# Performance work log

Measured on AMD Instinct MI355X. Metric: run time of the kernel, lower is better.

The kernel has to match this reference:

```python
import jax, jax.numpy as jnp
import numpy as np
import math

B, S, D, H = 4, 1024, 1024, 16
DK = D // H
K_INDEX = 5


def setup_inputs() -> dict:
    key = jax.random.key(0)
    ks = jax.random.split(key, 10)
    s = 0.02
    return {
        "query": jax.random.normal(ks[0], (B, S, D), jnp.float32),
        "key": jax.random.normal(ks[1], (B, S, D), jnp.float32),
        "values": jax.random.normal(ks[2], (B, S, D), jnp.float32),
        "lens": jax.random.randint(ks[3], (B,), 0, S),
        "Wq": jax.random.normal(ks[4], (D, D), jnp.float32) * s,  # shared q/k proj (kq_same=True)
        "bq": jnp.zeros((D,), jnp.float32),
        "Wv": jax.random.normal(ks[5], (D, D), jnp.float32) * s,
        "bv": jnp.zeros((D,), jnp.float32),
        "Wo": jax.random.normal(ks[6], (D, D), jnp.float32) * s,
        "bo": jnp.zeros((D,), jnp.float32),
        "gammas": jax.random.normal(ks[7], (H, 1, 1), jnp.float32) * 0.1,
        "ln_w": jnp.ones((D,), jnp.float32),
        "ln_b": jnp.zeros((D,), jnp.float32),
    }


def _split_heads(x):
    b, s, _ = x.shape
    return x.reshape(b, s, H, DK).transpose(0, 2, 1, 3)  # [B,H,S,DK]


def reference(query, key, values, lens, Wq, bq, Wv, bv, Wo, bo, gammas, ln_w, ln_b):
    # causal mask, peek_cur=False -> strict lower triangle; eval mode (no random masking)
    mask = jnp.tril(jnp.ones((S, S), bool), -1)[None, None]  # [1,1,S,S]

    q = _split_heads(query @ Wq.T + bq)
    k = _split_heads(key @ Wq.T + bq)   # kq_same: shared weights
    v = _split_heads(values @ Wv.T + bv)

    scores = jnp.einsum("bhid,bhjd->bhij", q, k) / math.sqrt(DK)
    NEG = jnp.finfo(scores.dtype).min

    # --- distance-decay term (no_grad in torch -> stop_gradient) ---
    s_ = jax.nn.softmax(jnp.where(mask, scores, NEG), axis=-1)
    distcum = jnp.cumsum(s_, axis=-1)
    disttotal = jnp.sum(s_, axis=-1, keepdims=True)
    idx = jnp.arange(S, dtype=scores.dtype)
    pos_effect = jnp.abs(idx[None, :] - idx[:, None])[None, None]  # |j - i|
    dist = jnp.sqrt(jnp.clip((disttotal - distcum) * pos_effect, 0.0, None))
    dist = jax.lax.stop_gradient(dist)

    gam = -jnp.abs(gammas)[None]  # [1,H,1,1]
    total_effect = jnp.clip(jnp.exp(dist * gam), 1e-5, 1e5)
    scores = scores * total_effect

    scores = jnp.where(mask, scores, NEG)
    p = jax.nn.softmax(scores, axis=-1)
    p = jnp.where(mask, p, 0.0)

    # maxout rescale (peek_cur=False)
    scale = jnp.minimum(1.0 / jnp.max(p, axis=-1, keepdims=True), 5.0)
    p = p * scale

    attn = jnp.einsum("bhij,bhjd->bhid", p, v)
    concat = attn.transpose(0, 2, 1, 3).reshape(B, S, D)
    attn_out = concat @ Wo.T + bo

    # k_select sparsification of the (post-softmax, maxout-scaled) scores
    sc_a = p[:, :, :K_INDEX, :]
    sc_b = p[:, :, K_INDEX:, :]
    kth = jax.lax.top_k(sc_b, K_INDEX)[0][..., -1:]  # k-th largest per row
    sc_b = jnp.where(sc_b >= kth, sc_b, NEG)
    sparse_scores = jax.nn.softmax(jnp.concatenate([sc_a, sc_b], axis=2), axis=-1)

    # residual (eval: dropout is identity) + LayerNorm
    y = query + attn_out
    mu = jnp.mean(y, axis=-1, keepdims=True)
    var = jnp.mean((y - mu) ** 2, axis=-1, keepdims=True)
    out = (y - mu) / jnp.sqrt(var + 1e-5) * ln_w + ln_b
    return (out, sparse_scores)
```

## Files before the change

### kernel.cpp

```cpp
#include <hip/hip_runtime.h>
#include <hip/hip_fp16.h>

#define Ssz 1024
#define Dsz 1024
#define Hsz 16
#define DKsz 64
#define Bsz 4
#define NEGI (-1.0e30f)
#define NEGD (-1.0e300)

typedef float f32x4 __attribute__((ext_vector_type(4)));
typedef float f32x2 __attribute__((ext_vector_type(2)));
typedef _Float16 f16x8 __attribute__((ext_vector_type(8)));
typedef _Float16 f16x4 __attribute__((ext_vector_type(4)));
typedef _Float16 f16x2 __attribute__((ext_vector_type(2)));

__device__ __forceinline__ float wmaxf(float x) {
#pragma unroll
  for (int o = 32; o; o >>= 1) x = fmaxf(x, __shfl_xor(x, o));
  return x;
}
__device__ __forceinline__ float wsumf(float x) {
#pragma unroll
  for (int o = 32; o; o >>= 1) x += __shfl_xor(x, o);
  return x;
}
__device__ __forceinline__ double wmaxd(double x) {
#pragma unroll
  for (int o = 32; o; o >>= 1) x = fmax(x, __shfl_xor(x, o));
  return x;
}
__device__ __forceinline__ double wsumd(double x) {
#pragma unroll
  for (int o = 32; o; o >>= 1) x += __shfl_xor(x, o);
  return x;
}
__device__ __forceinline__ int wmini(int x) {
#pragma unroll
  for (int o = 32; o; o >>= 1) x = min(x, __shfl_xor(x, o));
  return x;
}
__device__ __forceinline__ int sswz(int c) { return c ^ (((c >> 5) & 7) << 2); }
__device__ __forceinline__ int pswz(int c, int r) { return c ^ (r & 7) ^ ((c >> 3) & 7); }

__global__ __launch_bounds__(256) void wsplit_qv(
    const float* __restrict__ Wq, const float* __restrict__ Wv,
    __half* __restrict__ wqhi, __half* __restrict__ wqlo, __half* __restrict__ wvhi) {
  const size_t i = ((size_t)blockIdx.x * 256 + threadIdx.x) * 4;
  const f32x4 q = *(const f32x4*)(Wq + i);
  const f32x4 v = *(const f32x4*)(Wv + i);
  f16x4 hq, lq, hv;
#pragma unroll
  for (int e = 0; e < 4; e++) {
    const _Float16 h = (_Float16)q[e];
    hq[e] = h;
    lq[e] = (_Float16)(q[e] - (float)h);
    hv[e] = (_Float16)v[e];
  }
  *(f16x4*)((_Float16*)wqhi + i) = hq;
  *(f16x4*)((_Float16*)wqlo + i) = lq;
  *(f16x4*)((_Float16*)wvhi + i) = hv;
}

__global__ __launch_bounds__(256) void wsplit_o(
    const float* __restrict__ Wo, __half* __restrict__ wohi) {
  const size_t i = ((size_t)blockIdx.x * 256 + threadIdx.x) * 4;
  const f32x4 v = *(const f32x4*)(Wo + i);
  f16x4 hv;
#pragma unroll
  for (int e = 0; e < 4; e++) hv[e] = (_Float16)v[e];
  *(f16x4*)((_Float16*)wohi + i) = hv;
}

__global__ __launch_bounds__(256) void asplit_hl(
    const float* __restrict__ A, __half* __restrict__ hi, __half* __restrict__ lo) {
  const size_t i = ((size_t)blockIdx.x * 256 + threadIdx.x) * 4;
  const f32x4 v = *(const f32x4*)(A + i);
  f16x4 h, l;
#pragma unroll
  for (int e = 0; e < 4; e++) {
    const _Float16 hh = (_Float16)v[e];
    h[e] = hh;
    l[e] = (_Float16)(v[e] - (float)hh);
  }
  *(f16x4*)((_Float16*)hi + i) = h;
  *(f16x4*)((_Float16*)lo + i) = l;
}

__global__ __launch_bounds__(256) void asplit_h(
    const float* __restrict__ A, __half* __restrict__ hi) {
  const size_t i = ((size_t)blockIdx.x * 256 + threadIdx.x) * 4;
  const f32x4 v = *(const f32x4*)(A + i);
  f16x4 h;
#pragma unroll
  for (int e = 0; e < 4; e++) h[e] = (_Float16)v[e];
  *(f16x4*)((_Float16*)hi + i) = h;
}

__global__ __launch_bounds__(256) void gemm_qk(
    const __half* __restrict__ Ahi, const __half* __restrict__ Alo,
    const __half* __restrict__ wqhi, const __half* __restrict__ wqlo,
    const float* __restrict__ bias, __half* __restrict__ ohi, __half* __restrict__ olo) {
  const int w = threadIdx.x >> 6, lane = threadIdx.x & 63;
  const int quad = lane >> 4, l16 = lane & 15;
  const int m0 = blockIdx.x * 64 + w * 16;
  const int n0 = blockIdx.y * 64;
  f32x4 acc[4] = {};
  const size_t arow = (size_t)(m0 + l16) * Dsz;
  for (int k0 = 0; k0 < Dsz; k0 += 32) {
    const f16x8 ahi = *(const f16x8*)((const _Float16*)Ahi + arow + k0 + quad * 8);
    const f16x8 alo = *(const f16x8*)((const _Float16*)Alo + arow + k0 + quad * 8);
#pragma unroll
    for (int t = 0; t < 4; t++) {
      const size_t woff = (size_t)(n0 + t * 16 + l16) * Dsz + k0 + quad * 8;
      const f16x8 whi = *(const f16x8*)((const _Float16*)wqhi + woff);
      const f16x8 wlo = *(const f16x8*)((const _Float16*)wqlo + woff);
      acc[t] = __builtin_amdgcn_mfma_f32_16x16x32_f16(ahi, whi, acc[t], 0, 0, 0);
      acc[t] = __builtin_amdgcn_mfma_f32_16x16x32_f16(ahi, wlo, acc[t], 0, 0, 0);
      acc[t] = __builtin_amdgcn_mfma_f32_16x16x32_f16(alo, whi, acc[t], 0, 0, 0);
    }
  }
#pragma unroll
  for (int t = 0; t < 4; t++) {
    const int oc = n0 + t * 16 + l16;
    const float bv = bias[oc];
    const int hh = oc >> 6, dk = oc & 63;
#pragma unroll
    for (int r = 0; r < 4; r++) {
      const int mr = m0 + quad * 4 + r;
      const int bb = mr >> 10, ss = mr & 1023;
      const float v = acc[t][r] + bv;
      const size_t idx = ((size_t)(bb * Hsz + hh) * Ssz + ss) * DKsz + dk;
      const __half h = __float2half(v);
      ohi[idx] = h;
      olo[idx] = __float2half(v - __half2float(h));
    }
  }
}

__global__ __launch_bounds__(256) void gemm_v(
    const __half* __restrict__ Ahi, const __half* __restrict__ wvhi,
    const float* __restrict__ bias, __half* __restrict__ out_t) {
  const int w = threadIdx.x >> 6, lane = threadIdx.x & 63;
  const int quad = lane >> 4, l16 = lane & 15;
  const int m0 = blockIdx.x * 64 + w * 16;
  const int n0 = blockIdx.y * 64;
  f32x4 acc[4] = {};
  const size_t arow = (size_t)(m0 + l16) * Dsz;
  for (int k0 = 0; k0 < Dsz; k0 += 32) {
    const f16x8 ahi = *(const f16x8*)((const _Float16*)Ahi + arow + k0 + quad * 8);
#pragma unroll
    for (int t = 0; t < 4; t++) {
      const size_t woff = (size_t)(n0 + t * 16 + l16) * Dsz + k0 + quad * 8;
      const f16x8 whi = *(const f16x8*)((const _Float16*)wvhi + woff);
      acc[t] = __builtin_amdgcn_mfma_f32_16x16x32_f16(ahi, whi, acc[t], 0, 0, 0);
    }
  }
#pragma unroll
  for (int t = 0; t < 4; t++) {
    const int oc = n0 + t * 16 + l16;
    const float bv = bias[oc];
    const int hh = oc >> 6, dk = oc & 63;
#pragma unroll
    for (int r = 0; r < 4; r++) {
      const int mr = m0 + quad * 4 + r;
      const int bb = mr >> 10, ss = mr & 1023;
      out_t[((size_t)(bb * Hsz + hh) * DKsz + dk) * Ssz + ss] = __float2half(acc[t][r] + bv);
    }
  }
}

__global__ __launch_bounds__(256) void gemm_o(
    const __half* __restrict__ A, const __half* __restrict__ wohi,
    const float* __restrict__ bias, float* __restrict__ outf) {
  const int w = threadIdx.x >> 6, lane = threadIdx.x & 63;
  const int quad = lane >> 4, l16 = lane & 15;
  const int m0 = blockIdx.x * 64 + w * 16;
  const int n0 = blockIdx.y * 64;
  f32x4 acc[4] = {};
  const size_t arow = (size_t)(m0 + l16) * Dsz;
  for (int k0 = 0; k0 < Dsz; k0 += 32) {
    const f16x8 a = *(const f16x8*)(A + arow + k0 + quad * 8);
#pragma unroll
    for (int t = 0; t < 4; t++) {
      const size_t woff = (size_t)(n0 + t * 16 + l16) * Dsz + k0 + quad * 8;
      const f16x8 whi = *(const f16x8*)((const _Float16*)wohi + woff);
      acc[t] = __builtin_amdgcn_mfma_f32_16x16x32_f16(a, whi, acc[t], 0, 0, 0);
    }
  }
#pragma unroll
  for (int t = 0; t < 4; t++) {
    const int oc = n0 + t * 16 + l16;
    const float bv = bias[oc];
#pragma unroll
    for (int r = 0; r < 4; r++) {
      const int mr = m0 + quad * 4 + r;
      outf[(size_t)mr * Dsz + oc] = acc[t][r] + bv;
    }
  }
}


__global__ __launch_bounds__(256) void attn_scores(
    const __half* __restrict__ qhi, const __half* __restrict__ qlo,
    const __half* __restrict__ khi, const __half* __restrict__ klo,
    float* __restrict__ scores, int bh0) {
  const int w = threadIdx.x >> 6, lane = threadIdx.x & 63;
  const int quad = lane >> 4, l16 = lane & 15;
  const int lbh = blockIdx.y, bh = bh0 + lbh;
  for (int cc = 0; cc < 2; cc++) {
    const int chunk = cc ? (63 - (int)blockIdx.x) : (int)blockIdx.x;
    const int i0 = chunk * 16;
    const size_t qb = ((size_t)bh * Ssz + i0 + l16) * DKsz + quad * 8;
    const f16x8 ah0 = *(const f16x8*)(qhi + qb);
    const f16x8 ah1 = *(const f16x8*)(qhi + qb + 32);
    const f16x8 al0 = *(const f16x8*)(qlo + qb);
    const f16x8 al1 = *(const f16x8*)(qlo + qb + 32);
    float* dst = scores + ((size_t)lbh * Ssz + i0) * Ssz;
    for (int tt = 0; tt < 16; tt++) {
      const int n0 = (w + tt * 4) * 16;
      if (n0 > i0 + 14) continue;
      const size_t kb = ((size_t)bh * Ssz + n0 + l16) * DKsz + quad * 8;
      const f16x8 bh0v = *(const f16x8*)(khi + kb);
      const f16x8 bh1v = *(const f16x8*)(khi + kb + 32);
      const f16x8 bl0v = *(const f16x8*)(klo + kb);
      const f16x8 bl1v = *(const f16x8*)(klo + kb + 32);
      f32x4 accs = {};
      accs = __builtin_amdgcn_mfma_f32_16x16x32_f16(al0, bl0v, accs, 0, 0, 0);
      accs = __builtin_amdgcn_mfma_f32_16x16x32_f16(al1, bl1v, accs, 0, 0, 0);
      accs = __builtin_amdgcn_mfma_f32_16x16x32_f16(ah0, bl0v, accs, 0, 0, 0);
      accs = __builtin_amdgcn_mfma_f32_16x16x32_f16(ah1, bl1v, accs, 0, 0, 0);
      accs = __builtin_amdgcn_mfma_f32_16x16x32_f16(al0, bh0v, accs, 0, 0, 0);
      accs = __builtin_amdgcn_mfma_f32_16x16x32_f16(al1, bh1v, accs, 0, 0, 0);
      accs = __builtin_amdgcn_mfma_f32_16x16x32_f16(ah0, bh0v, accs, 0, 0, 0);
      accs = __builtin_amdgcn_mfma_f32_16x16x32_f16(ah1, bh1v, accs, 0, 0, 0);
#pragma unroll
      for (int r = 0; r < 4; r++)
        dst[(size_t)(quad * 4 + r) * Ssz + n0 + l16] = accs[r] * 0.125f;
    }
  }
}

__global__ __launch_bounds__(256) void attn_soft(
    float* __restrict__ scores, const float* __restrict__ gam,
    float* __restrict__ sparse, int bh0) {
  const int w = threadIdx.x >> 6, lane = threadIdx.x & 63;
  const int lbh = blockIdx.y, bh = bh0 + lbh;
  const int hidx = bh & 15;
  const float gf = -fabsf(gam[hidx]);
  const int jb = 2 * lane;
  for (int cc = 0; cc < 2; cc++) {
    const int chunk = cc ? (63 - (int)blockIdx.x) : (int)blockIdx.x;
    const int i0 = chunk * 16;
    for (int rr = 0; rr < 4; rr++) {
      const int gi = i0 + w * 4 + rr;
      const int nch = __builtin_amdgcn_readfirstlane((gi + 127) >> 7);
      float* rowp = scores + ((size_t)lbh * Ssz + gi) * Ssz;
      float xf[16];
      float m1 = NEGI;
#pragma unroll
      for (int e = 0; e < 8; e++) {
        if (e < nch) {
          const int j0 = 128 * e + jb;
          const f32x2 t = *(const f32x2*)(rowp + j0);
          xf[2 * e] = t[0];
          xf[2 * e + 1] = t[1];
          if (j0 < gi) m1 = fmaxf(m1, t[0]);
          if (j0 + 1 < gi) m1 = fmaxf(m1, t[1]);
        }
      }
      m1 = wmaxf(m1);
      float s[16];
#pragma unroll
      for (int k = 0; k < 16; k++) s[k] = 0.f;
#pragma unroll
      for (int e = 0; e < 8; e++) {
        if (e < nch) {
          const int j0 = 128 * e + jb;
          if (j0 < gi) s[2 * e] = __expf(xf[2 * e] - m1);
          if (j0 + 1 < gi) s[2 * e + 1] = __expf(xf[2 * e + 1] - m1);
        }
      }
      float tot[8];
#pragma unroll
      for (int e = 0; e < 8; e++) {
        if (e < nch) {
          const float q2 = s[2 * e] + s[2 * e + 1];
          float v = __shfl_down(q2, 1);
          if (lane == 63) v = 0.f;
#pragma unroll
          for (int o = 1; o < 64; o <<= 1) {
            const float t = __shfl_down(v, o);
            if (lane + o < 64) v += t;
          }
          tot[e] = __shfl(q2 + v, 0);
          const float t1 = v;
          const float t0e = v + s[2 * e + 1];
          s[2 * e] = t0e;
          s[2 * e + 1] = t1;
        }
      }
      float csum = 0.f;
#pragma unroll
      for (int e = 7; e >= 0; e--) {
        if (e < nch) {
          s[2 * e] += csum;
          s[2 * e + 1] += csum;
          csum += tot[e];
        }
      }
      const float ls = csum;
      const float invls = (ls > 0.f) ? 1.0f / ls : 0.f;
      float ys[16];
      float m2 = NEGI;
#pragma unroll
      for (int k = 0; k < 16; k++) ys[k] = NEGI;
#pragma unroll
      for (int e = 0; e < 8; e++) {
        if (e < nch) {
#pragma unroll
          for (int i = 0; i < 2; i++) {
            const int j = 128 * e + jb + i;
            if (j < gi) {
              const float pe = (float)(gi - j);
              const float tn = s[2 * e + i] * invls;
              const float tl = tn > 0.f ? tn * pe : 0.f;
              float te = __expf(gf * sqrtf(tl));
              te = te < 1e-5f ? 1e-5f : te;
              const float vv = xf[2 * e + i] * te;
              ys[2 * e + i] = vv;
              m2 = fmaxf(m2, vv);
            }
          }
        }
      }
      m2 = wmaxf(m2);
      float xs[16];
#pragma unroll
      for (int k = 0; k < 16; k++) xs[k] = 0.f;
      float ls3 = 0.f, mev = 0.f;
#pragma unroll
      for (int e = 0; e < 8; e++) {
        if (e < nch) {
#pragma unroll
          for (int i = 0; i < 2; i++) {
            const int j = 128 * e + jb + i;
            if (j < gi) {
              const float ev = __expf(ys[2 * e + i] - m2);
              xs[2 * e + i] = ev;
              ls3 += ev;
              mev = fmaxf(mev, ev);
            }
          }
        }
      }
      ls3 = wsumf(ls3);
      mev = wmaxf(mev);
      const float inv2 = (ls3 > 0.f) ? 1.0f / ls3 : 0.f;
      const float mp = mev * inv2;
      const float scl = (mp > 0.f) ? fminf(1.0f / mp, 5.0f) : 5.0f;
      const float c2 = inv2 * scl;
#pragma unroll
      for (int k = 0; k < 16; k++) xs[k] *= c2;
      const float m3 = mp * scl;
      {
        _Float16* prow = (_Float16*)rowp;
#pragma unroll
        for (int e = 0; e < 8; e++) {
          f16x2 hp;
          hp[0] = (_Float16)xs[2 * e];
          hp[1] = (_Float16)xs[2 * e + 1];
          *(f16x2*)(prow + 128 * e + jb) = hp;
        }
      }

      float* dst = sparse + ((size_t)bh * Ssz + gi) * Ssz;
      if (gi < 5) {
        float o4[16];
        float ls4 = 0.f;
#pragma unroll
        for (int k = 0; k < 16; k++) {
          const float ev = expf(xs[k] - m3);
          o4[k] = ev;
          ls4 += ev;
        }
        const float inv3 = 1.0f / fmaxf(wsumf(ls4), 1e-30f);
#pragma unroll
        for (int e = 0; e < 8; e++) {
          f32x2 st;
          st[0] = o4[2 * e] * inv3;
          st[1] = o4[2 * e + 1] * inv3;
          *(f32x2*)(dst + 128 * e + jb) = st;
        }
      } else {
        float m5 = 0.f, m6 = 0.f;
        {
          unsigned int removed = 0;
          for (int r6 = 0; r6 < 6; r6++) {
            float lm = NEGI;
#pragma unroll
            for (int k = 0; k < 16; k++)
              if (!((removed >> k) & 1)) lm = fmaxf(lm, ys[k]);
            const float m = wmaxf(lm);
            const unsigned long long bal = __ballot(lm == m);
            const int src = __ffsll(bal) - 1;
            int rem_k = 0;
#pragma unroll
            for (int k = 15; k >= 0; k--)
              if (!((removed >> k) & 1) && ys[k] == m) rem_k = k;
            if (lane == src) removed |= 1u << rem_k;
            if (r6 == 4) m5 = m;
            if (r6 == 5) m6 = m;
          }
        }
        const float bstar = 0.5f * (m5 + m6);
        const float ETA = 6e-5f;
        const float wlo = m6 - 0.1f, whi = m5 + 0.1f;
        float md[16];
        float mn = 0.f;
#pragma unroll
        for (int e = 0; e < 8; e++) {
          md[2 * e] = 0.f;
          md[2 * e + 1] = 0.f;
          if (e < nch) {
#pragma unroll
            for (int i = 0; i < 2; i++) {
              const int j = 128 * e + jb + i;
              const int k = 2 * e + i;
              if (j < gi && ys[k] >= wlo && ys[k] <= whi) {
                const float pe = (float)(gi - j);
                const float t0 = fmaxf(s[k] * invls, 0.f);
                float telo = __expf(gf * sqrtf(fmaxf(t0 - ETA, 0.f) * pe));
                telo = fminf(fmaxf(telo, 1e-5f), 1.0f);
                float tehi = __expf(gf * sqrtf((t0 + ETA) * pe));
                tehi = fminf(fmaxf(tehi, 1e-5f), 1.0f);
                md[k] = fminf(fabsf(xf[k]) * (telo - tehi) + 2e-4f, 0.04f);
                mn = fmaxf(mn, md[k]);
              }
            }
          }
        }
        mn = wmaxf(mn);
        float cnt = 0.f;
        unsigned int mK = 0, mA = 0;
#pragma unroll
        for (int e = 0; e < 8; e++) {
          if (e < nch) {
#pragma unroll
            for (int i = 0; i < 2; i++) {
              const int j = 128 * e + jb + i;
              const int k = 2 * e + i;
              if (j < gi) {
                const float margin = fminf(1.5f * (md[k] + mn) + 1e-4f, 0.06f);
                if (ys[k] > bstar + margin) {
                  mK |= 1u << k; cnt += 1.f;
                } else if (!(ys[k] < bstar - margin)) {
                  mA |= 1u << k; cnt += 2048.f;
                }
              }
            }
          }
        }
        cnt = wsumf(cnt);
        const float cA = floorf(cnt * (1.0f / 2048.0f));
        const float cK = cnt - 2048.0f * cA;
        float vvf[16];
        float vK = 0.f, vA = 0.f;
#pragma unroll
        for (int k = 0; k < 16; k++) {
          vvf[k] = 0.f;
          if (((mK | mA) >> k) & 1) {
            const float val = __expf(xs[k] - m3);
            vvf[k] = val;
            if ((mK >> k) & 1) vK += val; else vA += val;
          }
        }
        vK = wsumf(vK); vA = wsumf(vA);
        const float vbar = (cA > 0.5f) ? vA / cA : 0.f;
        const float Zhat = vK + (5.0f - cK) * vbar;
        const float invZ = (Zhat > 0.f) ? 1.0f / Zhat : 0.f;
#pragma unroll
        for (int e = 0; e < 8; e++) {
          f32x2 st;
#pragma unroll
          for (int i = 0; i < 2; i++) {
            const int k = 2 * e + i;
            const bool isK = (mK >> k) & 1;
            const bool isA = (mA >> k) & 1;
            st[i] = isK ? vvf[k] * invZ : isA ? 0.5f * vvf[k] * invZ : 0.f;
          }
          *(f32x2*)(dst + 128 * e + jb) = st;
        }
      }
    }
  }
}

__global__ __launch_bounds__(256) void attn_pv(
    const float* __restrict__ scoresP, const __half* __restrict__ vt,
    __half* __restrict__ attn_c, int bh0) {
  const int w = threadIdx.x >> 6, lane = threadIdx.x & 63;
  const int quad = lane >> 4, l16 = lane & 15;
  const int lbh = blockIdx.y, bh = bh0 + lbh;
  const int hidx = bh & 15, bidx = bh >> 4;
  const _Float16* pb = (const _Float16*)scoresP;
  const int dk0 = w * 16;
  for (int cc = 0; cc < 2; cc++) {
    const int chunk = cc ? (63 - (int)blockIdx.x) : (int)blockIdx.x;
    const int i0 = chunk * 16;
    const int kmax = (i0 + 15 + 31) & ~31;
    f32x4 acc = {};
    const size_t prow = ((size_t)lbh * Ssz + i0 + l16) * 2048;
    const size_t vrow = ((size_t)bh * DKsz + dk0 + l16) * Ssz;
    for (int k0 = 0; k0 < kmax; k0 += 32) {
      const f16x8 a = *(const f16x8*)(pb + prow + k0 + quad * 8);
      const f16x8 b = *(const f16x8*)(vt + vrow + k0 + quad * 8);
      acc = __builtin_amdgcn_mfma_f32_16x16x32_f16(a, b, acc, 0, 0, 0);
    }
#pragma unroll
    for (int r = 0; r < 4; r++) {
      const int ss = i0 + quad * 4 + r;
      attn_c[((size_t)bidx * Ssz + ss) * Dsz + hidx * DKsz + dk0 + l16] = __float2half(acc[r]);
    }
  }
}

__global__ __launch_bounds__(256) void attn_kernel(
    const __half* __restrict__ qhi, const __half* __restrict__ qlo,
    const __half* __restrict__ khi, const __half* __restrict__ klo,
    const __half* __restrict__ vt, const float* __restrict__ gam,
    __half* __restrict__ attn_c, float* __restrict__ sparse) {
  __shared__ __align__(16) float sc[16 * 1024];
  const int w = threadIdx.x >> 6, lane = threadIdx.x & 63;
  const int quad = lane >> 4, l16 = lane & 15;
  const int bh = blockIdx.y, i0 = blockIdx.x * 16;
  const int hidx = bh & 15, bidx = bh >> 4;
  _Float16* pbase = (_Float16*)sc;

  {
    const size_t qb = ((size_t)bh * Ssz + i0 + l16) * DKsz + quad * 8;
    const f16x8 ah0 = *(const f16x8*)(qhi + qb);
    const f16x8 ah1 = *(const f16x8*)(qhi + qb + 32);
    const f16x8 al0 = *(const f16x8*)(qlo + qb);
    const f16x8 al1 = *(const f16x8*)(qlo + qb + 32);
    for (int tt = 0; tt < 16; tt++) {
      const int n0 = (w + tt * 4) * 16;
      const size_t kb = ((size_t)bh * Ssz + n0 + l16) * DKsz + quad * 8;
      const f16x8 bh0 = *(const f16x8*)(khi + kb);
      const f16x8 bh1 = *(const f16x8*)(khi + kb + 32);
      const f16x8 bl0 = *(const f16x8*)(klo + kb);
      const f16x8 bl1 = *(const f16x8*)(klo + kb + 32);
      f32x4 accs = {};
      accs = __builtin_amdgcn_mfma_f32_16x16x32_f16(al0, bl0, accs, 0, 0, 0);
      accs = __builtin_amdgcn_mfma_f32_16x16x32_f16(al1, bl1, accs, 0, 0, 0);
      accs = __builtin_amdgcn_mfma_f32_16x16x32_f16(ah0, bl0, accs, 0, 0, 0);
      accs = __builtin_amdgcn_mfma_f32_16x16x32_f16(ah1, bl1, accs, 0, 0, 0);
      accs = __builtin_amdgcn_mfma_f32_16x16x32_f16(al0, bh0, accs, 0, 0, 0);
      accs = __builtin_amdgcn_mfma_f32_16x16x32_f16(al1, bh1, accs, 0, 0, 0);
      accs = __builtin_amdgcn_mfma_f32_16x16x32_f16(ah0, bh0, accs, 0, 0, 0);
      accs = __builtin_amdgcn_mfma_f32_16x16x32_f16(ah1, bh1, accs, 0, 0, 0);
      const int pc = sswz(n0 + l16);
#pragma unroll
      for (int r = 0; r < 4; r++)
        sc[(quad * 4 + r) * 1024 + pc] = accs[r] * 0.125f;
    }
  }
  __syncthreads();

  {
    const double g = -fabs((double)gam[hidx]);
    for (int rr = 0; rr < 4; rr++) {
      const int r = w * 4 + rr, gi = i0 + r;
      float xf[16];
#pragma unroll
// ... 203 lines not shown
      const f16x8 a = *(const f16x8*)(pbase + l16 * 2048 + pswz(cch, l16) * 8);
      const f16x8 b =
          *(const f16x8*)(vt + ((size_t)bh * DKsz + dk0 + l16) * Ssz + k0 + quad * 8);
      acc = __builtin_amdgcn_mfma_f32_16x16x32_f16(a, b, acc, 0, 0, 0);
    }
#pragma unroll
    for (int r = 0; r < 4; r++) {
      const int ss = i0 + quad * 4 + r;
      attn_c[((size_t)bidx * Ssz + ss) * Dsz + hidx * DKsz + dk0 + l16] = __float2half(acc[r]);
    }
  }
}

__global__ __launch_bounds__(256) void ln_kernel(
    const float* __restrict__ query, const float* __restrict__ attn_out,
    const float* __restrict__ ln_w, const float* __restrict__ ln_b,
    float* __restrict__ out) {
  __shared__ float red[8];
  const int n = blockIdx.x, t = threadIdx.x;
  const int w = t >> 6, lane = t & 63;
  float y[4];
  float s = 0.f, s2 = 0.f;
#pragma unroll
  for (int k = 0; k < 4; k++) {
    const int j = t + k * 256;
    const float v = query[(size_t)n * Dsz + j] + attn_out[(size_t)n * Dsz + j];
    y[k] = v;
    s += v;
    s2 += v * v;
  }
  s = wsumf(s);
  s2 = wsumf(s2);
  if (lane == 0) { red[w] = s; red[4 + w] = s2; }
  __syncthreads();
  s = red[0] + red[1] + red[2] + red[3];
  s2 = red[4] + red[5] + red[6] + red[7];
  const float mu = s * (1.0f / 1024.0f);
  const float var = fmaxf(s2 * (1.0f / 1024.0f) - mu * mu, 0.0f);
  const float rs = rsqrtf(var + 1e-5f);
#pragma unroll
  for (int k = 0; k < 4; k++) {
    const int j = t + k * 256;
    out[(size_t)n * Dsz + j] = (y[k] - mu) * rs * ln_w[j] + ln_b[j];
  }
}

extern "C" void kernel_launch(void* const* d_in, const int* in_sizes, int n_in,
                              void* d_out, int out_size, void* d_ws, size_t ws_size,
                              hipStream_t stream) {
  (void)in_sizes; (void)n_in; (void)out_size;
  const float* query = (const float*)d_in[0];
  const float* key = (const float*)d_in[1];
  const float* values = (const float*)d_in[2];
  const float* Wq = (const float*)d_in[4];
  const float* bq = (const float*)d_in[5];
  const float* Wv = (const float*)d_in[6];
  const float* bv = (const float*)d_in[7];
  const float* Wo = (const float*)d_in[8];
  const float* bo = (const float*)d_in[9];
  const float* gam = (const float*)d_in[10];
  const float* lnw = (const float*)d_in[11];
  const float* lnb = (const float*)d_in[12];

  char* ws = (char*)d_ws;
  const size_t MB = 1024u * 1024u;
  const size_t MB8 = 8u * MB;
  __half* qhi = (__half*)ws;
  __half* qlo = (__half*)(ws + 1 * MB8);
  __half* khi = (__half*)(ws + 2 * MB8);
  __half* klo = (__half*)(ws + 3 * MB8);
  __half* vt = (__half*)(ws + 4 * MB8);
  __half* attn_c = (__half*)(ws + 5 * MB8);
  float* attn_out = (float*)ws;
  float* scores = (float*)(ws + 6 * MB8);

  __half* wqhi = (__half*)(ws + 5 * MB8);
  __half* wqlo = (__half*)(ws + 5 * MB8 + 2 * MB);
  __half* wvhi = (__half*)(ws + 5 * MB8 + 4 * MB);
  __half* wohi = (__half*)(ws + 2 * MB8);

  float* out = (float*)d_out;
  float* sparse = out + (size_t)Bsz * Ssz * Dsz;

  __half* sa_hi = (__half*)((char*)sparse);
  __half* sa_lo = (__half*)((char*)sparse + 8 * MB);
  __half* sv = (__half*)((char*)sparse + 16 * MB);

  const size_t avail = (ws_size > 6 * MB8) ? (ws_size - 6 * MB8) : 0;
  int cbh = 0;
  if (avail >= 64u * 4u * MB) cbh = 64;
  else if (avail >= 32u * 4u * MB) cbh = 32;
  else if (avail >= 16u * 4u * MB) cbh = 16;
  else if (avail >= 8u * 4u * MB) cbh = 8;

  const dim3 gg(64, 16), gb(256);
  wsplit_qv<<<1024, 256, 0, stream>>>(Wq, Wv, wqhi, wqlo, wvhi);
  asplit_hl<<<4096, 256, 0, stream>>>(query, sa_hi, sa_lo);
  gemm_qk<<<gg, gb, 0, stream>>>(sa_hi, sa_lo, wqhi, wqlo, bq, qhi, qlo);
  asplit_hl<<<4096, 256, 0, stream>>>(key, sa_hi, sa_lo);
  gemm_qk<<<gg, gb, 0, stream>>>(sa_hi, sa_lo, wqhi, wqlo, bq, khi, klo);
  asplit_h<<<4096, 256, 0, stream>>>(values, sv);
  gemm_v<<<gg, gb, 0, stream>>>(sv, wvhi, bv, vt);
  if (cbh > 0) {
    for (int bh0 = 0; bh0 < Bsz * Hsz; bh0 += cbh) {
      attn_scores<<<dim3(32, cbh), 256, 0, stream>>>(qhi, qlo, khi, klo, scores, bh0);
      attn_soft<<<dim3(32, cbh), 256, 0, stream>>>(scores, gam, sparse, bh0);
      attn_pv<<<dim3(32, cbh), 256, 0, stream>>>(scores, vt, attn_c, bh0);
    }
  } else {
    attn_kernel<<<dim3(64, 64), 256, 0, stream>>>(qhi, qlo, khi, klo, vt, gam, attn_c, sparse);
  }
  wsplit_o<<<1024, 256, 0, stream>>>(Wo, wohi);
  gemm_o<<<gg, gb, 0, stream>>>(attn_c, wohi, bo, attn_out);
  ln_kernel<<<(Bsz * Ssz), 256, 0, stream>>>(query, attn_out, lnw, lnb, out);
}
```

Before: 1.274 ms.

## Merge conversion kernels, batch Q/K projections, process two rows per softmax pass

Folds the five fp32-to-fp16 split kernels into one launch and runs the Q and K projections as a single gemm_qk launch using blockIdx.z. The softmax/sparsify kernel now handles two rows per wavefront iteration, pairing their shuffle reductions and scans so independent work can interleave and hide latency. The aim is fewer launches and better instruction-level parallelism in attn_soft. The cost is roughly double the register use in attn_soft, which may lower occupancy or cause spills.

```diff
diff --git a/kernel.cpp b/kernel.cpp
--- a/kernel.cpp
+++ b/kernel.cpp
@@ -25,6 +25,24 @@
   for (int o = 32; o; o >>= 1) x += __shfl_xor(x, o);
   return x;
 }
+__device__ __forceinline__ void wmaxf2(float& a, float& b) {
+#pragma unroll
+  for (int o = 32; o; o >>= 1) {
+    const float ta = __shfl_xor(a, o);
+    const float tb = __shfl_xor(b, o);
+    a = fmaxf(a, ta);
+    b = fmaxf(b, tb);
+  }
+}
+__device__ __forceinline__ void wsumf2(float& a, float& b) {
+#pragma unroll
+  for (int o = 32; o; o >>= 1) {
+    const float ta = __shfl_xor(a, o);
+    const float tb = __shfl_xor(b, o);
+    a += ta;
+    b += tb;
+  }
+}
 __device__ __forceinline__ double wmaxd(double x) {
 #pragma unroll
   for (int o = 32; o; o >>= 1) x = fmax(x, __shfl_xor(x, o));
@@ -43,23 +61,44 @@
 __device__ __forceinline__ int sswz(int c) { return c ^ (((c >> 5) & 7) << 2); }
 __device__ __forceinline__ int pswz(int c, int r) { return c ^ (r & 7) ^ ((c >> 3) & 7); }
 
-__global__ __launch_bounds__(256) void wsplit_qv(
+__device__ __forceinline__ void cvt_hl(const float* __restrict__ src,
+                                       _Float16* __restrict__ hi,
+                                       _Float16* __restrict__ lo, int blk) {
+  const size_t i = ((size_t)blk * 256 + threadIdx.x) * 4;
+  const f32x4 v = *(const f32x4*)(src + i);
+  f16x4 h, l;
+#pragma unroll
+  for (int e = 0; e < 4; e++) {
+    const _Float16 hh = (_Float16)v[e];
+    h[e] = hh;
+    l[e] = (_Float16)(v[e] - (float)hh);
+  }
+  *(f16x4*)(hi + i) = h;
+  *(f16x4*)(lo + i) = l;
+}
+__device__ __forceinline__ void cvt_h(const float* __restrict__ src,
+                                      _Float16* __restrict__ hi, int blk) {
+  const size_t i = ((size_t)blk * 256 + threadIdx.x) * 4;
+  const f32x4 v = *(const f32x4*)(src + i);
+  f16x4 h;
+#pragma unroll
+  for (int e = 0; e < 4; e++) h[e] = (_Float16)v[e];
+  *(f16x4*)(hi + i) = h;
+}
+
+__global__ __launch_bounds__(256) void precvt(
     const float* __restrict__ Wq, const float* __restrict__ Wv,
-    __half* __restrict__ wqhi, __half* __restrict__ wqlo, __half* __restrict__ wvhi) {
-  const size_t i = ((size_t)blockIdx.x * 256 + threadIdx.x) * 4;
-  const f32x4 q = *(const f32x4*)(Wq + i);
-  const f32x4 v = *(const f32x4*)(Wv + i);
-  f16x4 hq, lq, hv;
-#pragma unroll
-  for (int e = 0; e < 4; e++) {
-    const _Float16 h = (_Float16)q[e];
-    hq[e] = h;
-    lq[e] = (_Float16)(q[e] - (float)h);
-    hv[e] = (_Float16)v[e];
-  }
-  *(f16x4*)((_Float16*)wqhi + i) = hq;
-  *(f16x4*)((_Float16*)wqlo + i) = lq;
-  *(f16x4*)((_Float16*)wvhi + i) = hv;
+    const float* __restrict__ query, const float* __restrict__ key,
+    const float* __restrict__ values,
+    __half* __restrict__ wqhi, __half* __restrict__ wqlo, __half* __restrict__ wvhi,
+    __half* __restrict__ q_hi, __half* __restrict__ q_lo,
+    __half* __restrict__ k_hi, __half* __restrict__ k_lo, __half* __restrict__ v_h) {
+  const int b = blockIdx.x;
+  if (b < 1024) cvt_hl(Wq, (_Float16*)wqhi, (_Float16*)wqlo, b);
+  else if (b < 2048) cvt_h(Wv, (_Float16*)wvhi, b - 1024);
+  else if (b < 6144) cvt_hl(query, (_Float16*)q_hi, (_Float16*)q_lo, b - 2048);
+  else if (b < 10240) cvt_hl(key, (_Float16*)k_hi, (_Float16*)k_lo, b - 6144);
+  else cvt_h(values, (_Float16*)v_h, b - 10240);
 }
 
 __global__ __launch_bounds__(256) void wsplit_o(
@@ -72,35 +111,18 @@
   *(f16x4*)((_Float16*)wohi + i) = hv;
 }
 
-__global__ __launch_bounds__(256) void asplit_hl(
-    const float* __restrict__ A, __half* __restrict__ hi, __half* __restrict__ lo) {
-  const size_t i = ((size_t)blockIdx.x * 256 + threadIdx.x) * 4;
-  const f32x4 v = *(const f32x4*)(A + i);
-  f16x4 h, l;
-#pragma unroll
-  for (int e = 0; e < 4; e++) {
-    const _Float16 hh = (_Float16)v[e];
-    h[e] = hh;
-    l[e] = (_Float16)(v[e] - (float)hh);
-  }
-  *(f16x4*)((_Float16*)hi + i) = h;
-  *(f16x4*)((_Float16*)lo + i) = l;
-}
-
-__global__ __launch_bounds__(256) void asplit_h(
-    const float* __restrict__ A, __half* __restrict__ hi) {
-  const size_t i = ((size_t)blockIdx.x * 256 + threadIdx.x) * 4;
-  const f32x4 v = *(const f32x4*)(A + i);
-  f16x4 h;
-#pragma unroll
-  for (int e = 0; e < 4; e++) h[e] = (_Float16)v[e];
-  *(f16x4*)((_Float16*)hi + i) = h;
-}
-
 __global__ __launch_bounds__(256) void gemm_qk(
-    const __half* __restrict__ Ahi, const __half* __restrict__ Alo,
+    const __half* __restrict__ A0hi, const __half* __restrict__ A0lo,
+    const __half* __restrict__ A1hi, const __half* __restrict__ A1lo,
     const __half* __restrict__ wqhi, const __half* __restrict__ wqlo,
-    const float* __restrict__ bias, __half* __restrict__ ohi, __half* __restrict__ olo) {
+    const float* __restrict__ bias,
+    __half* __restrict__ o0hi, __half* __restrict__ o0lo,
+    __half* __restrict__ o1hi, __half* __restrict__ o1lo) {
+  const int z = blockIdx.z;
+  const _Float16* Ahi = (const _Float16*)(z ? A1hi : A0hi);
+  const _Float16* Alo = (const _Float16*)(z ? A1lo : A0lo);
+  __half* ohi = z ? o1hi : o0hi;
+  __half* olo = z ? o1lo : o0lo;
   const int w = threadIdx.x >> 6, lane = threadIdx.x & 63;
   const int quad = lane >> 4, l16 = lane & 15;
   const int m0 = blockIdx.x * 64 + w * 16;
@@ -108,8 +130,8 @@
   f32x4 acc[4] = {};
   const size_t arow = (size_t)(m0 + l16) * Dsz;
   for (int k0 = 0; k0 < Dsz; k0 += 32) {
-    const f16x8 ahi = *(const f16x8*)((const _Float16*)Ahi + arow + k0 + quad * 8);
-    const f16x8 alo = *(const f16x8*)((const _Float16*)Alo + arow + k0 + quad * 8);
+    const f16x8 ahi = *(const f16x8*)(Ahi + arow + k0 + quad * 8);
+    const f16x8 alo = *(const f16x8*)(Alo + arow + k0 + quad * 8);
 #pragma unroll
     for (int t = 0; t < 4; t++) {
       const size_t woff = (size_t)(n0 + t * 16 + l16) * Dsz + k0 + quad * 8;
@@ -252,244 +274,342 @@
   for (int cc = 0; cc < 2; cc++) {
     const int chunk = cc ? (63 - (int)blockIdx.x) : (int)blockIdx.x;
     const int i0 = chunk * 16;
-    for (int rr = 0; rr < 4; rr++) {
-      const int gi = i0 + w * 4 + rr;
-      const int nch = __builtin_amdgcn_readfirstlane((gi + 127) >> 7);
-      float* rowp = scores + ((size_t)lbh * Ssz + gi) * Ssz;
-      float xf[16];
-      float m1 = NEGI;
+    for (int rp = 0; rp < 2; rp++) {
+      const int gia = i0 + w * 4 + 2 * rp;
+      const int gib = gia + 1;
+      const int nch = __builtin_amdgcn_readfirstlane((gib + 127) >> 7);
+      float* rowpa = scores + ((size_t)lbh * Ssz + gia) * Ssz;
+      float* rowpb = rowpa + Ssz;
+
+      float xf[2][16];
+      float m1a = NEGI, m1b = NEGI;
 #pragma unroll
       for (int e = 0; e < 8; e++) {
         if (e < nch) {
           const int j0 = 128 * e + jb;
-          const f32x2 t = *(const f32x2*)(rowp + j0);
-          xf[2 * e] = t[0];
-          xf[2 * e + 1] = t[1];
-          if (j0 < gi) m1 = fmaxf(m1, t[0]);
-          if (j0 + 1 < gi) m1 = fmaxf(m1, t[1]);
-        }
-      }
-      m1 = wmaxf(m1);
-      float s[16];
-#pragma unroll
-      for (int k = 0; k < 16; k++) s[k] = 0.f;
+          const f32x2 ta = *(const f32x2*)(rowpa + j0);
+          const f32x2 tb = *(const f32x2*)(rowpb + j0);
+          xf[0][2 * e] = ta[0]; xf[0][2 * e + 1] = ta[1];
+          xf[1][2 * e] = tb[0]; xf[1][2 * e + 1] = tb[1];
+          if (j0 < gia) m1a = fmaxf(m1a, ta[0]);
+          if (j0 + 1 < gia) m1a = fmaxf(m1a, ta[1]);
+          if (j0 < gib) m1b = fmaxf(m1b, tb[0]);
+          if (j0 + 1 < gib) m1b = fmaxf(m1b, tb[1]);
+        }
+      }
+      wmaxf2(m1a, m1b);
+      float s[2][16];
+#pragma unroll
+      for (int k = 0; k < 16; k++) { s[0][k] = 0.f; s[1][k] = 0.f; }
 #pragma unroll
       for (int e = 0; e < 8; e++) {
         if (e < nch) {
           const int j0 = 128 * e + jb;
-          if (j0 < gi) s[2 * e] = __expf(xf[2 * e] - m1);
-          if (j0 + 1 < gi) s[2 * e + 1] = __expf(xf[2 * e + 1] - m1);
-        }
-      }
-      float tot[8];
+          if (j0 < gia) s[0][2 * e] = __expf(xf[0][2 * e] - m1a);
+          if (j0 + 1 < gia) s[0][2 * e + 1] = __expf(xf[0][2 * e + 1] - m1a);
+          if (j0 < gib) s[1][2 * e] = __expf(xf[1][2 * e] - m1b);
+          if (j0 + 1 < gib) s[1][2 * e + 1] = __expf(xf[1][2 * e + 1] - m1b);
+        }
+      }
+      float tot[2][8];
 #pragma unroll
       for (int e = 0; e < 8; e++) {
         if (e < nch) {
-          const float q2 = s[2 * e] + s[2 * e + 1];
-          float v = __shfl_down(q2, 1);
-          if (lane == 63) v = 0.f;
+          const float qa = s[0][2 * e] + s[0][2 * e + 1];
+          const float qb = s[1][2 * e] + s[1][2 * e + 1];
+          float va = __shfl_down(qa, 1);
+          float vb = __shfl_down(qb, 1);
+          if (lane == 63) { va = 0.f; vb = 0.f; }
 #pragma unroll
           for (int o = 1; o < 64; o <<= 1) {
-            const float t = __shfl_down(v, o);
-            if (lane + o < 64) v += t;
-          }
-          tot[e] = __shfl(q2 + v, 0);
-          const float t1 = v;
-          const float t0e = v + s[2 * e + 1];
-          s[2 * e] = t0e;
-          s[2 * e + 1] = t1;
-        }
-      }
-      float csum = 0.f;
+            const float ta = __shfl_down(va, o);
+            const float tb = __shfl_down(vb, o);
+            if (lane + o < 64) { va += ta; vb += tb; }
+          }
+          tot[0][e] = __shfl(qa + va, 0);
+          tot[1][e] = __shfl(qb + vb, 0);
+          const float t0a = va + s[0][2 * e + 1];
+          const float t0b = vb + s[1][2 * e + 1];
+          s[0][2 * e] = t0a; s[0][2 * e + 1] = va;
+          s[1][2 * e] = t0b; s[1][2 * e + 1] = vb;
+        }
+      }
+      float csa = 0.f, csb = 0.f;
 #pragma unroll
       for (int e = 7; e >= 0; e--) {
         if (e < nch) {
-          s[2 * e] += csum;
-          s[2 * e + 1] += csum;
-          csum += tot[e];
-        }
-      }
-      const float ls = csum;
-      const float invls = (ls > 0.f) ? 1.0f / ls : 0.f;
-      float ys[16];
-      float m2 = NEGI;
-#pragma unroll
-      for (int k = 0; k < 16; k++) ys[k] = NEGI;
+          s[0][2 * e] += csa; s[0][2 * e + 1] += csa; csa += tot[0][e];
+          s[1][2 * e] += csb; s[1][2 * e + 1] += csb; csb += tot[1][e];
+        }
+      }
+      const float invlsa = (csa > 0.f) ? 1.0f / csa : 0.f;
+      const float invlsb = (csb > 0.f) ? 1.0f / csb : 0.f;
+      float ys[2][16];
+      float m2a = NEGI, m2b = NEGI;
+#pragma unroll
+      for (int k = 0; k < 16; k++) { ys[0][k] = NEGI; ys[1][k] = NEGI; }
 #pragma unroll
       for (int e = 0; e < 8; e++) {
         if (e < nch) {
 #pragma unroll
           for (int i = 0; i < 2; i++) {
             const int j = 128 * e + jb + i;
-            if (j < gi) {
-              const float pe = (float)(gi - j);
-              const float tn = s[2 * e + i] * invls;
+            const int k = 2 * e + i;
+            if (j < gia) {
+              const float pe = (float)(gia - j);
+              const float tn = s[0][k] * invlsa;
               const float tl = tn > 0.f ? tn * pe : 0.f;
               float te = __expf(gf * sqrtf(tl));
               te = te < 1e-5f ? 1e-5f : te;
-              const float vv = xf[2 * e + i] * te;
-              ys[2 * e + i] = vv;
-              m2 = fmaxf(m2, vv);
+              const float vv = xf[0][k] * te;
+              ys[0][k] = vv;
+              m2a = fmaxf(m2a, vv);
             }
-          }
-        }
-      }
-      m2 = wmaxf(m2);
-      float xs[16];
-#pragma unroll
-      for (int k = 0; k < 16; k++) xs[k] = 0.f;
-      float ls3 = 0.f, mev = 0.f;
+            if (j < gib) {
+              const float pe = (float)(gib - j);
+              const float tn = s[1][k] * invlsb;
+              const float tl = tn > 0.f ? tn * pe : 0.f;
+              float te = __expf(gf * sqrtf(tl));
+              te = te < 1e-5f ? 1e-5f : te;
+              const float vv = xf[1][k] * te;
+              ys[1][k] = vv;
+              m2b = fmaxf(m2b, vv);
+            }
+          }
+        }
+      }
+      wmaxf2(m2a, m2b);
+      float xs[2][16];
+#pragma unroll
+      for (int k = 0; k < 16; k++) { xs[0][k] = 0.f; xs[1][k] = 0.f; }
+      float lsa = 0.f, lsb = 0.f, meva = 0.f, mevb = 0.f;
 #pragma unroll
       for (int e = 0; e < 8; e++) {
         if (e < nch) {
 #pragma unroll
           for (int i = 0; i < 2; i++) {
             const int j = 128 * e + jb + i;
-            if (j < gi) {
-              const float ev = __expf(ys[2 * e + i] - m2);
-              xs[2 * e + i] = ev;
-              ls3 += ev;
-              mev = fmaxf(mev, ev);
+            const int k = 2 * e + i;
+            if (j < gia) {
+              const float ev = __expf(ys[0][k] - m2a);
+              xs[0][k] = ev;
+              lsa += ev;
+              meva = fmaxf(meva, ev);
             }
-          }
-        }
-      }
-      ls3 = wsumf(ls3);
-      mev = wmaxf(mev);
-      const float inv2 = (ls3 > 0.f) ? 1.0f / ls3 : 0.f;
-      const float mp = mev * inv2;
-      const float scl = (mp > 0.f) ? fminf(1.0f / mp, 5.0f) : 5.0f;
-      const float c2 = inv2 * scl;
-#pragma unroll
-      for (int k = 0; k < 16; k++) xs[k] *= c2;
-      const float m3 = mp * scl;
+            if (j < gib) {
+              const float ev = __expf(ys[1][k] - m2b);
+              xs[1][k] = ev;
+              lsb += ev;
+              mevb = fmaxf(mevb, ev);
+            }
+          }
+        }
+      }
+      wsumf2(lsa, lsb);
+      wmaxf2(meva, mevb);
+      const float inv2a = (lsa > 0.f) ? 1.0f / lsa : 0.f;
+      const float inv2b = (lsb > 0.f) ? 1.0f / lsb : 0.f;
+      const float mpa = meva * inv2a;
+      const float mpb = mevb * inv2b;
+      const float scla = (mpa > 0.f) ? fminf(1.0f / mpa, 5.0f) : 5.0f;
+      const float sclb = (mpb > 0.f) ? fminf(1.0f / mpb, 5.0f) : 5.0f;
+      const float c2a = inv2a * scla, c2b = inv2b * sclb;
+#pragma unroll
+      for (int k = 0; k < 16; k++) { xs[0][k] *= c2a; xs[1][k] *= c2b; }
+      const float m3a = mpa * scla;
+      const float m3b = mpb * sclb;
       {
-        _Float16* prow = (_Float16*)rowp;
+        _Float16* prowa = (_Float16*)rowpa;
+        _Float16* prowb = (_Float16*)rowpb;
 #pragma unroll
         for (int e = 0; e < 8; e++) {
-          f16x2 hp;
-          hp[0] = (_Float16)xs[2 * e];
-          hp[1] = (_Float16)xs[2 * e + 1];
-          *(f16x2*)(prow + 128 * e + jb) = hp;
-        }
-      }
-
-      float* dst = sparse + ((size_t)bh * Ssz + gi) * Ssz;
-      if (gi < 5) {
-        float o4[16];
-        float ls4 = 0.f;
-#pragma unroll
-        for (int k = 0; k < 16; k++) {
-          const float ev = expf(xs[k] - m3);
-          o4[k] = ev;
-          ls4 += ev;
-        }
-        const float inv3 = 1.0f / fmaxf(wsumf(ls4), 1e-30f);
-#pragma unroll
-        for (int e = 0; e < 8; e++) {
-          f32x2 st;
-          st[0] = o4[2 * e] * inv3;
-          st[1] = o4[2 * e + 1] * inv3;
-          *(f32x2*)(dst + 128 * e + jb) = st;
-        }
-      } else {
-        float m5 = 0.f, m6 = 0.f;
-        {
-          unsigned int removed = 0;
-          for (int r6 = 0; r6 < 6; r6++) {
-            float lm = NEGI;
-#pragma unroll
-            for (int k = 0; k < 16; k++)
-              if (!((removed >> k) & 1)) lm = fmaxf(lm, ys[k]);
-            const float m = wmaxf(lm);
-            const unsigned long long bal = __ballot(lm == m);
-            const int src = __ffsll(bal) - 1;
-            int rem_k = 0;
-#pragma unroll
-            for (int k = 15; k >= 0; k--)
-              if (!((removed >> k) & 1) && ys[k] == m) rem_k = k;
-            if (lane == src) removed |= 1u << rem_k;
-            if (r6 == 4) m5 = m;
-            if (r6 == 5) m6 = m;
-          }
-        }
-        const float bstar = 0.5f * (m5 + m6);
-        const float ETA = 6e-5f;
-        const float wlo = m6 - 0.1f, whi = m5 + 0.1f;
-        float md[16];
-        float mn = 0.f;
-#pragma unroll
-        for (int e = 0; e < 8; e++) {
-          md[2 * e] = 0.f;
-          md[2 * e + 1] = 0.f;
-          if (e < nch) {
-#pragma unroll
-            for (int i = 0; i < 2; i++) {
-              const int j = 128 * e + jb + i;
-              const int k = 2 * e + i;
-              if (j < gi && ys[k] >= wlo && ys[k] <= whi) {
-                const float pe = (float)(gi - j);
-                const float t0 = fmaxf(s[k] * invls, 0.f);
-                float telo = __expf(gf * sqrtf(fmaxf(t0 - ETA, 0.f) * pe));
-                telo = fminf(fmaxf(telo, 1e-5f), 1.0f);
-                float tehi = __expf(gf * sqrtf((t0 + ETA) * pe));
-                tehi = fminf(fmaxf(tehi, 1e-5f), 1.0f);
-                md[k] = fminf(fabsf(xf[k]) * (telo - tehi) + 2e-4f, 0.04f);
-                mn = fmaxf(mn, md[k]);
+          f16x2 ha, hb;
+          ha[0] = (_Float16)xs[0][2 * e]; ha[1] = (_Float16)xs[0][2 * e + 1];
+          hb[0] = (_Float16)xs[1][2 * e]; hb[1] = (_Float16)xs[1][2 * e + 1];
+          *(f16x2*)(prowa + 128 * e + jb) = ha;
+          *(f16x2*)(prowb + 128 * e + jb) = hb;
+        }
+      }
+
+      float* dsta = sparse + ((size_t)bh * Ssz + gia) * Ssz;
+      float* dstb = dsta + Ssz;
+      if (gia < 5) {
+#pragma unroll
+        for (int p = 0; p < 2; p++) {
+          const int gi = p ? gib : gia;
+          if (gi < 5) {
+            const float m3p = p ? m3b : m3a;
+            float* dst = p ? dstb : dsta;
+            float o4[16];
+            float ls4 = 0.f;
+#pragma unroll
+            for (int k = 0; k < 16; k++) {
+              const float ev = expf(xs[p][k] - m3p);
+              o4[k] = ev;
+              ls4 += ev;
+            }
+            const float inv3 = 1.0f / fmaxf(wsumf(ls4), 1e-30f);
+#pragma unroll
+            for (int e = 0; e < 8; e++) {
+              f32x2 st;
+              st[0] = o4[2 * e] * inv3;
+              st[1] = o4[2 * e + 1] * inv3;
+              *(f32x2*)(dst + 128 * e + jb) = st;
+            }
+          }
+        }
+      }
+      float m5a = 0.f, m6a = 0.f, m5b = 0.f, m6b = 0.f;
+      {
+        unsigned int ra = 0, rb = 0;
+        for (int r6 = 0; r6 < 6; r6++) {
+          float lma = NEGI, lmb = NEGI;
+#pragma unroll
+          for (int k = 0; k < 16; k++) {
+            if (!((ra >> k) & 1)) lma = fmaxf(lma, ys[0][k]);
+            if (!((rb >> k) & 1)) lmb = fmaxf(lmb, ys[1][k]);
+          }
+          float ma = lma, mb = lmb;
+          wmaxf2(ma, mb);
+          const unsigned long long bala = __ballot(lma == ma);
+          const unsigned long long balb = __ballot(lmb == mb);
+          const int srca = __ffsll(bala) - 1;
+          const int srcb = __ffsll(balb) - 1;
+          int rka = 0, rkb = 0;
+#pragma unroll
+          for (int k = 15; k >= 0; k--) {
+            if (!((ra >> k) & 1) && ys[0][k] == ma) rka = k;
+            if (!((rb >> k) & 1) && ys[1][k] == mb) rkb = k;
+          }
+          if (lane == srca) ra |= 1u << rka;
+          if (lane == srcb) rb |= 1u << rkb;
+          if (r6 == 4) { m5a = ma; m5b = mb; }
+          if (r6 == 5) { m6a = ma; m6b = mb; }
+        }
+      }
+      const float bstara = 0.5f * (m5a + m6a);
+      const float bstarb = 0.5f * (m5b + m6b);
+      const float ETA = 6e-5f;
+      const float wloa = m6a - 0.1f, whia = m5a + 0.1f;
+      const float wlob = m6b - 0.1f, whib = m5b + 0.1f;
+      float md[2][16];
+      float mna = 0.f, mnb = 0.f;
+#pragma unroll
+      for (int e = 0; e < 8; e++) {
+        md[0][2 * e] = 0.f; md[0][2 * e + 1] = 0.f;
+        md[1][2 * e] = 0.f; md[1][2 * e + 1] = 0.f;
+        if (e < nch) {
+#pragma unroll
+          for (int i = 0; i < 2; i++) {
+            const int j = 128 * e + jb + i;
+            const int k = 2 * e + i;
+            if (j < gia && ys[0][k] >= wloa && ys[0][k] <= whia) {
+              const float pe = (float)(gia - j);
+              const float t0 = fmaxf(s[0][k] * invlsa, 0.f);
+              float telo = __expf(gf * sqrtf(fmaxf(t0 - ETA, 0.f) * pe));
+              telo = fminf(fmaxf(telo, 1e-5f), 1.0f);
+              float tehi = __expf(gf * sqrtf((t0 + ETA) * pe));
+              tehi = fminf(fmaxf(tehi, 1e-5f), 1.0f);
+              md[0][k] = fminf(fabsf(xf[0][k]) * (telo - tehi) + 2e-4f, 0.04f);
+              mna = fmaxf(mna, md[0][k]);
+            }
+            if (j < gib && ys[1][k] >= wlob && ys[1][k] <= whib) {
+              const float pe = (float)(gib - j);
+              const float t0 = fmaxf(s[1][k] * invlsb, 0.f);
+              float telo = __expf(gf * sqrtf(fmaxf(t0 - ETA, 0.f) * pe));
+              telo = fminf(fmaxf(telo, 1e-5f), 1.0f);
+              float tehi = __expf(gf * sqrtf((t0 + ETA) * pe));
+              tehi = fminf(fmaxf(tehi, 1e-5f), 1.0f);
+              md[1][k] = fminf(fabsf(xf[1][k]) * (telo - tehi) + 2e-4f, 0.04f);
+              mnb = fmaxf(mnb, md[1][k]);
+            }
+          }
+        }
+      }
+      wmaxf2(mna, mnb);
+      float cnta = 0.f, cntb = 0.f;
+      unsigned int mKa = 0, mAa = 0, mKb = 0, mAb = 0;
+#pragma unroll
+      for (int e = 0; e < 8; e++) {
+        if (e < nch) {
+#pragma unroll
+          for (int i = 0; i < 2; i++) {
+            const int j = 128 * e + jb + i;
+            const int k = 2 * e + i;
+            if (j < gia) {
+              const float margin = fminf(1.5f * (md[0][k] + mna) + 1e-4f, 0.06f);
+              if (ys[0][k] > bstara + margin) {
+                mKa |= 1u << k; cnta += 1.f;
+              } else if (!(ys[0][k] < bstara - margin)) {
+                mAa |= 1u << k; cnta += 2048.f;
               }
             }
-          }
-        }
-        mn = wmaxf(mn);
-        float cnt = 0.f;
-        unsigned int mK = 0, mA = 0;
-#pragma unroll
-        for (int e = 0; e < 8; e++) {
-          if (e < nch) {
-#pragma unroll
-            for (int i = 0; i < 2; i++) {
-              const int j = 128 * e + jb + i;
-              const int k = 2 * e + i;
-              if (j < gi) {
-                const float margin = fminf(1.5f * (md[k] + mn) + 1e-4f, 0.06f);
-                if (ys[k] > bstar + margin) {
-                  mK |= 1u << k; cnt += 1.f;
-                } else if (!(ys[k] < bstar - margin)) {
-                  mA |= 1u << k; cnt += 2048.f;
-                }
+            if (j < gib) {
+              const float margin = fminf(1.5f * (md[1][k] + mnb) + 1e-4f, 0.06f);
+              if (ys[1][k] > bstarb + margin) {
+                mKb |= 1u << k; cntb += 1.f;
+              } else if (!(ys[1][k] < bstarb - margin)) {
+                mAb |= 1u << k; cntb += 2048.f;
               }
             }
           }
         }
-        cnt = wsumf(cnt);
-        const float cA = floorf(cnt * (1.0f / 2048.0f));
-        const float cK = cnt - 2048.0f * cA;
-        float vvf[16];
-        float vK = 0.f, vA = 0.f;
-#pragma unroll
-        for (int k = 0; k < 16; k++) {
-          vvf[k] = 0.f;
-          if (((mK | mA) >> k) & 1) {
-            const float val = __expf(xs[k] - m3);
-            vvf[k] = val;
-            if ((mK >> k) & 1) vK += val; else vA += val;
-          }
-        }
-        vK = wsumf(vK); vA = wsumf(vA);
-        const float vbar = (cA > 0.5f) ? vA / cA : 0.f;
-        const float Zhat = vK + (5.0f - cK) * vbar;
-        const float invZ = (Zhat > 0.f) ? 1.0f / Zhat : 0.f;
-#pragma unroll
-        for (int e = 0; e < 8; e++) {
+      }
+      wsumf2(cnta, cntb);
+      const float cAa = floorf(cnta * (1.0f / 2048.0f));
+      const float cKa = cnta - 2048.0f * cAa;
+      const float cAb = floorf(cntb * (1.0f / 2048.0f));
+      const float cKb = cntb - 2048.0f * cAb;
+      float vKa = 0.f, vAa = 0.f, vKb = 0.f, vAb = 0.f;
+#pragma unroll
+      for (int k = 0; k < 16; k++) {
+        {
+          const bool live = ((mKa | mAa) >> k) & 1;
+          const float val = live ? __expf(xs[0][k] - m3a) : 0.f;
+          xs[0][k] = val;
+          if ((mKa >> k) & 1) vKa += val;
+          else if (live) vAa += val;
+        }
+        {
+          const bool live = ((mKb | mAb) >> k) & 1;
+          const float val = live ? __expf(xs[1][k] - m3b) : 0.f;
+          xs[1][k] = val;
+          if ((mKb >> k) & 1) vKb += val;
+          else if (live) vAb += val;
+        }
+      }
+      wsumf2(vKa, vKb);
+      wsumf2(vAa, vAb);
+      const float vbara = (cAa > 0.5f) ? vAa / cAa : 0.f;
+      const float vbarb = (cAb > 0.5f) ? vAb / cAb : 0.f;
+      const float Zhata = vKa + (5.0f - cKa) * vbara;
+      const float Zhatb = vKb + (5.0f - cKb) * vbarb;
+      const float invZa = (Zhata > 0.f) ? 1.0f / Zhata : 0.f;
+      const float invZb = (Zhatb > 0.f) ? 1.0f / Zhatb : 0.f;
+      const bool wra = (gia >= 5), wrb = (gib >= 5);
+#pragma unroll
+      for (int e = 0; e < 8; e++) {
+        if (wra) {
           f32x2 st;
 #pragma unroll
           for (int i = 0; i < 2; i++) {
             const int k = 2 * e + i;
-            const bool isK = (mK >> k) & 1;
-            const bool isA = (mA >> k) & 1;
-            st[i] = isK ? vvf[k] * invZ : isA ? 0.5f * vvf[k] * invZ : 0.f;
-          }
-          *(f32x2*)(dst + 128 * e + jb) = st;
+            const bool isK = (mKa >> k) & 1;
+            const bool isA = (mAa >> k) & 1;
+            st[i] = isK ? xs[0][k] * invZa : isA ? 0.5f * xs[0][k] * invZa : 0.f;
+          }
+          *(f32x2*)(dsta + 128 * e + jb) = st;
+        }
+        if (wrb) {
+          f32x2 st;
+#pragma unroll
+          for (int i = 0; i < 2; i++) {
+            const int k = 2 * e + i;
+            const bool isK = (mKb >> k) & 1;
+            const bool isA = (mAb >> k) & 1;
+            st[i] = isK ? xs[1][k] * invZb : isA ? 0.5f * xs[1][k] * invZb : 0.f;
+          }
+          *(f32x2*)(dstb + 128 * e + jb) = st;
         }
       }
     }
@@ -859,9 +979,11 @@
   float* out = (float*)d_out;
   float* sparse = out + (size_t)Bsz * Ssz * Dsz;
 
-  __half* sa_hi = (__half*)((char*)sparse);
-  __half* sa_lo = (__half*)((char*)sparse + 8 * MB);
-  __half* sv = (__half*)((char*)sparse + 16 * MB);
+  __half* q_hi = (__half*)((char*)sparse);
+  __half* q_lo = (__half*)((char*)sparse + 8 * MB);
+  __half* k_hi = (__half*)((char*)sparse + 16 * MB);
+  __half* k_lo = (__half*)((char*)sparse + 24 * MB);
+  __half* v_h = (__half*)((char*)sparse + 32 * MB);
 
   const size_t avail = (ws_size > 6 * MB8) ? (ws_size - 6 * MB8) : 0;
   int cbh = 0;
@@ -871,13 +993,11 @@
   else if (avail >= 8u * 4u * MB) cbh = 8;
 
   const dim3 gg(64, 16), gb(256);
-  wsplit_qv<<<1024, 256, 0, stream>>>(Wq, Wv, wqhi, wqlo, wvhi);
-  asplit_hl<<<4096, 256, 0, stream>>>(query, sa_hi, sa_lo);
-  gemm_qk<<<gg, gb, 0, stream>>>(sa_hi, sa_lo, wqhi, wqlo, bq, qhi, qlo);
-  asplit_hl<<<4096, 256, 0, stream>>>(key, sa_hi, sa_lo);
-  gemm_qk<<<gg, gb, 0, stream>>>(sa_hi, sa_lo, wqhi, wqlo, bq, khi, klo);
-  asplit_h<<<4096, 256, 0, stream>>>(values, sv);
-  gemm_v<<<gg, gb, 0, stream>>>(sv, wvhi, bv, vt);
+  precvt<<<14336, 256, 0, stream>>>(Wq, Wv, query, key, values, wqhi, wqlo, wvhi,
+                                    q_hi, q_lo, k_hi, k_lo, v_h);
+  gemm_qk<<<dim3(64, 16, 2), gb, 0, stream>>>(q_hi, q_lo, k_hi, k_lo, wqhi, wqlo,
+                                              bq, qhi, qlo, khi, klo);
+  gemm_v<<<gg, gb, 0, stream>>>(v_h, wvhi, bv, vt);
   if (cbh > 0) {
     for (int bh0 = 0; bh0 < Bsz * Hsz; bh0 += cbh) {
       attn_scores<<<dim3(32, cbh), 256, 0, stream>>>(qhi, qlo, khi, klo, scores, bh0);
```

Result: no change. 1.296 ms (+1.7%).
